# Optimization experiments

Hardware: AMD Instinct MI355X
Metric: run time of the kernel (lower is better)

The kernel has to match this reference:

```python
import jax, jax.numpy as jnp
import numpy as np
import math

B, L, D = 2, 2048, 512
D_INNER, D_STATE, D_CONV = 2 * D, 16, 4
DT_RANK = math.ceil(D / 16)  # 32


def setup_inputs() -> dict:
    key = jax.random.key(0)
    ks = jax.random.split(key, 9)
    s = 0.02
    x = jax.random.normal(ks[0], (B, L, D), dtype=jnp.float32)
    W_in = jax.random.normal(ks[1], (D, 2 * D_INNER), dtype=jnp.float32) * s
    conv_w = jax.random.normal(ks[2], (D_INNER, D_CONV), dtype=jnp.float32) * s
    conv_b = jnp.zeros((D_INNER,), dtype=jnp.float32)
    W_x = jax.random.normal(ks[3], (D_INNER, DT_RANK + 2 * D_STATE), dtype=jnp.float32) * s
    W_dt = jax.random.normal(ks[4], (DT_RANK, D_INNER), dtype=jnp.float32) * s
    b_dt = jax.random.normal(ks[5], (D_INNER,), dtype=jnp.float32) * s
    # S4D-real init: A = -[1..d_state] per channel
    A_log = jnp.log(jnp.broadcast_to(jnp.arange(1, D_STATE + 1, dtype=jnp.float32), (D_INNER, D_STATE)))
    D_param = jnp.ones((D_INNER,), dtype=jnp.float32)
    W_out = jax.random.normal(ks[6], (D_INNER, D), dtype=jnp.float32) * s
    return {"x": x, "W_in": W_in, "conv_w": conv_w, "conv_b": conv_b,
            "W_x": W_x, "W_dt": W_dt, "b_dt": b_dt, "A_log": A_log,
            "D_param": D_param, "W_out": W_out}


def _mamba(x, W_in, conv_w, conv_b, W_x, W_dt, b_dt, A_log, D_param, W_out):
    # in_proj -> [u, z]
    xz = jnp.einsum('bld,de->ble', x, W_in)
    u, z = jnp.split(xz, 2, axis=-1)  # each (B, L, d_inner)
    # depthwise causal conv1d along L
    u_c = jnp.transpose(u, (0, 2, 1))  # (B, d_inner, L)
    kern = conv_w[:, None, :]          # (d_inner, 1, d_conv)
    u_c = jax.lax.conv_general_dilated(
        u_c, kern, window_strides=(1,), padding=[(D_CONV - 1, 0)],
        feature_group_count=D_INNER,
        dimension_numbers=('NCH', 'OIH', 'NCH')) + conv_b[None, :, None]
    u = jax.nn.silu(jnp.transpose(u_c, (0, 2, 1)))  # (B, L, d_inner)
    # input-dependent dt, B, C
    x_dbl = jnp.einsum('bld,de->ble', u, W_x)
    dt_r = x_dbl[..., :DT_RANK]
    Bm = x_dbl[..., DT_RANK:DT_RANK + D_STATE]          # (B, L, d_state)
    Cm = x_dbl[..., DT_RANK + D_STATE:]                  # (B, L, d_state)
    dt = jax.nn.softplus(jnp.einsum('blr,rd->bld', dt_r, W_dt) + b_dt)  # (B, L, d_inner)
    A = -jnp.exp(A_log)  # (d_inner, d_state)

    def step(h, inp):
        dt_t, B_t, C_t, u_t = inp  # (B,d_inner), (B,d_state), (B,d_state), (B,d_inner)
        dA = jnp.exp(dt_t[:, :, None] * A)                      # (B, d_inner, d_state)
        h = h * dA + (dt_t * u_t)[:, :, None] * B_t[:, None, :]
        y = jnp.einsum('bds,bs->bd', h, C_t)
        return h, y

    h0 = jnp.zeros((B, D_INNER, D_STATE), dtype=x.dtype)
    xs = (jnp.transpose(dt, (1, 0, 2)), jnp.transpose(Bm, (1, 0, 2)),
          jnp.transpose(Cm, (1, 0, 2)), jnp.transpose(u, (1, 0, 2)))
    _, ys = jax.lax.scan(step, h0, xs)
    y = jnp.transpose(ys, (1, 0, 2)) + u * D_param  # (B, L, d_inner)
    y = y * jax.nn.silu(z)
    return jnp.einsum('bld,de->ble', y, W_out)


def reference(x, W_in, conv_w, conv_b, W_x, W_dt, b_dt, A_log, D_param, W_out):
    # MambaLayer.forward (eval): out = x + drop_path(mamba(x)); drop_path == Identity at eval
    return x + _mamba(x, W_in, conv_w, conv_b, W_x, W_dt, b_dt, A_log, D_param, W_out)
```

## Files before the change

### kernel.cpp

```cpp
#include <hip/hip_runtime.h>
#include <math.h>

#define BB 2
#define LL 2048
#define DD 512
#define DIN 1024
#define DXZ 2048
#define DSTATE 16
#define DTRANK 32
#define NDBL 64
#define ML (BB*LL)
#define LC2 64
#define NCH2 (LL/LC2)
#define CP 68

typedef __bf16 bf16_t;
typedef bf16_t bf16x8 __attribute__((ext_vector_type(8)));
typedef bf16_t bf16x4 __attribute__((ext_vector_type(4)));
typedef float f32x4 __attribute__((ext_vector_type(4)));

#define GBK 32
#define GBKP 40

__device__ __forceinline__ float fast_silu(float x) {
  return x * __builtin_amdgcn_rcpf(1.f + __builtin_amdgcn_exp2f(-1.44269504f * x));
}

template <int TM, int TN, int MODE, int CT>
__launch_bounds__(256)
__global__ void gemm_mfma(const bf16_t* __restrict__ A,
                          const bf16_t* __restrict__ Bt,
                          float* __restrict__ C, int ldc,
                          int M, int N, int K,
                          const float* __restrict__ aux) {
  __shared__ __align__(16) bf16_t As[TM * GBKP];
  __shared__ __align__(16) bf16_t Bs[TN * GBKP];
  const int tid = threadIdx.x;
  const int wid = tid >> 6, lane = tid & 63;
  const int q = lane >> 4, ln = lane & 15;
  constexpr int WM = TM / 2, WN = TN / 2;
  constexpr int FM = WM / 16, FN = WN / 16;
  const int wm = (wid >> 1) * WM, wn = (wid & 1) * WN;
  const int mBase = blockIdx.y * TM, nBase = blockIdx.x * TN;

  f32x4 acc[FM][FN] = {};

  for (int k0 = 0; k0 < K; k0 += GBK) {
#pragma unroll
    for (int i = 0; i < TM * GBK / (256 * 8); i++) {
      const int slot = tid + i * 256;
      const int m = slot >> 2, k8 = (slot & 3) * 8;
      *(bf16x8*)&As[m * GBKP + k8] =
          *(const bf16x8*)&A[(size_t)(mBase + m) * K + k0 + k8];
    }
#pragma unroll
    for (int i = 0; i < TN * GBK / (256 * 8); i++) {
      const int slot = tid + i * 256;
      const int n = slot >> 2, k8 = (slot & 3) * 8;
      *(bf16x8*)&Bs[n * GBKP + k8] =
          *(const bf16x8*)&Bt[(size_t)(nBase + n) * K + k0 + k8];
    }
    __syncthreads();
    bf16x8 af[FM], bfr[FN];
#pragma unroll
    for (int i = 0; i < FM; i++)
      af[i] = *(const bf16x8*)&As[(wm + i * 16 + ln) * GBKP + q * 8];
#pragma unroll
    for (int j = 0; j < FN; j++)
      bfr[j] = *(const bf16x8*)&Bs[(wn + j * 16 + ln) * GBKP + q * 8];
#pragma unroll
    for (int i = 0; i < FM; i++)
#pragma unroll
      for (int j = 0; j < FN; j++)
        acc[i][j] = __builtin_amdgcn_mfma_f32_16x16x32_bf16(
            af[i], bfr[j], acc[i][j], 0, 0, 0);
    __syncthreads();
  }

#pragma unroll
  for (int i = 0; i < FM; i++) {
    const int m0 = mBase + wm + i * 16 + q * 4;
#pragma unroll
    for (int j = 0; j < FN; j++) {
      const int n = nBase + wn + j * 16 + ln;
      if (CT == 1) {
        *(f32x4*)&C[(size_t)n * ldc + m0] = acc[i][j];
      } else {
#pragma unroll
        for (int r = 0; r < 4; r++) {
          float v = acc[i][j][r];
          if (MODE == 2) v += aux[(size_t)(m0 + r) * ldc + n];
          C[(size_t)(m0 + r) * ldc + n] = v;
        }
      }
    }
  }
}

__global__ void cast_bf16(const float* __restrict__ in, bf16_t* __restrict__ out,
                          int n4) {
  const int i = blockIdx.x * 256 + threadIdx.x;
  if (i >= n4) return;
  const float4 v = ((const float4*)in)[i];
  bf16x4 o = {(bf16_t)v.x, (bf16_t)v.y, (bf16_t)v.z, (bf16_t)v.w};
  ((bf16x4*)out)[i] = o;
}

__launch_bounds__(256)
__global__ void transpose_cast(const float* __restrict__ in, bf16_t* __restrict__ out,
                               int R, int C) {
  __shared__ float T[64][65];
  const int t = threadIdx.x;
  const int rB = blockIdx.y * 64, cB = blockIdx.x * 64;
  {
    const int r = t >> 4, c4 = (t & 15) * 4;
#pragma unroll
    for (int i = 0; i < 4; i++) {
      const float4 v = *(const float4*)&in[(size_t)(rB + r + i * 16) * C + cB + c4];
      T[r + i * 16][c4] = v.x;
      T[r + i * 16][c4 + 1] = v.y;
      T[r + i * 16][c4 + 2] = v.z;
      T[r + i * 16][c4 + 3] = v.w;
    }
  }
  __syncthreads();
  {
    const int c = t >> 2;
#pragma unroll
    for (int i = 0; i < 4; i++) {
      const int r0 = (t & 3) * 16 + i * 4;
      bf16x4 o = {(bf16_t)T[r0][c], (bf16_t)T[r0 + 1][c],
                  (bf16_t)T[r0 + 2][c], (bf16_t)T[r0 + 3][c]};
      *(bf16x4*)&out[(size_t)(cB + c) * R + rB + r0] = o;
    }
  }
}

template <int MODE, int AT, int CT>
__launch_bounds__(256)
__global__ void gemm_tiled(const float* __restrict__ A, int lda,
                           const float* __restrict__ B, int ldb,
                           float* __restrict__ C, int ldc,
                           int M, int N, int K,
                           const float* __restrict__ aux) {
  __shared__ float As[16][68];
  __shared__ float Bs[16][68];

  const int tid = threadIdx.x;
  const int tx = tid & 15, ty = tid >> 4;
  const int mBase = blockIdx.y * 64;
  const int nBase = blockIdx.x * 64;

  float acc[4][4] = {};

  for (int k0 = 0; k0 < K; k0 += 16) {
#pragma unroll
    for (int i = 0; i < 4; i++) {
      int idx = tid + i * 256;
      if (AT == 0) {
        int m = idx >> 4, kk = idx & 15;
        As[kk][m] = A[(size_t)(mBase + m) * lda + k0 + kk];
      } else {
        int kk = idx >> 6, m = idx & 63;
        As[kk][m] = A[(size_t)(k0 + kk) * lda + mBase + m];
      }
    }
#pragma unroll
    for (int i = 0; i < 4; i++) {
      int idx = tid + i * 256;
      int kk = idx >> 6, n = idx & 63;
      Bs[kk][n] = B[(size_t)(k0 + kk) * ldb + nBase + n];
    }
    __syncthreads();
#pragma unroll
    for (int kk = 0; kk < 16; kk++) {
      const float4 a4 = *reinterpret_cast<const float4*>(&As[kk][ty * 4]);
      const float4 b4 = *reinterpret_cast<const float4*>(&Bs[kk][tx * 4]);
      const float a[4] = {a4.x, a4.y, a4.z, a4.w};
      const float b[4] = {b4.x, b4.y, b4.z, b4.w};
#pragma unroll
      for (int i = 0; i < 4; i++)
#pragma unroll
        for (int j = 0; j < 4; j++) acc[i][j] = fmaf(a[i], b[j], acc[i][j]);
    }
    __syncthreads();
  }

  if (CT == 0) {
#pragma unroll
    for (int i = 0; i < 4; i++) {
      const int m = mBase + ty * 4 + i;
      const int n0 = nBase + tx * 4;
      float v[4];
#pragma unroll
      for (int j = 0; j < 4; j++) {
        float x = acc[i][j];
        if (MODE == 1) {
          x += aux[n0 + j];
          x = (x > 20.f) ? x
              : 0.69314718f * __builtin_amdgcn_logf(
                    1.f + __builtin_amdgcn_exp2f(x * 1.44269504f));
        }
        v[j] = x;
      }
      *reinterpret_cast<float4*>(&C[(size_t)m * ldc + n0]) =
          make_float4(v[0], v[1], v[2], v[3]);
    }
  } else {
    const int m0 = mBase + ty * 4;
#pragma unroll
    for (int j = 0; j < 4; j++) {
      const int n = nBase + tx * 4 + j;
      float v[4];
#pragma unroll
      for (int i = 0; i < 4; i++) {
        float x = acc[i][j];
        if (MODE == 1) {
          x += aux[n];
          x = (x > 20.f) ? x
              : 0.69314718f * __builtin_amdgcn_logf(
                    1.f + __builtin_amdgcn_exp2f(x * 1.44269504f));
        }
        v[i] = x;
      }
      *reinterpret_cast<float4*>(&C[(size_t)n * ldc + m0]) =
          make_float4(v[0], v[1], v[2], v[3]);
    }
  }
}

__launch_bounds__(256)
__global__ void conv_silu_T(const float* __restrict__ xzT,
                            const float* __restrict__ conv_w,
                            const float* __restrict__ conv_b,
                            float* __restrict__ uT) {
  const int idx = blockIdx.x * 256 + threadIdx.x;
  const int d = idx >> 10;
  const int ml0 = (idx & 1023) * 4;
  const int l0 = ml0 & (LL - 1);
  const float* row = xzT + (size_t)d * ML + ml0;
  const float4 Bv = *reinterpret_cast<const float4*>(row);
  float4 Av = make_float4(0.f, 0.f, 0.f, 0.f);
  if (l0 != 0) Av = *reinterpret_cast<const float4*>(row - 4);
  const float w0 = conv_w[d * 4 + 0], w1 = conv_w[d * 4 + 1];
  const float w2 = conv_w[d * 4 + 2], w3 = conv_w[d * 4 + 3];
  const float bias = conv_b[d];
  float o[4];
  o[0] = bias + w0 * Av.y + w1 * Av.z + w2 * Av.w + w3 * Bv.x;
  o[1] = bias + w0 * Av.z + w1 * Av.w + w2 * Bv.x + w3 * Bv.y;
  o[2] = bias + w0 * Av.w + w1 * Bv.x + w2 * Bv.y + w3 * Bv.z;
  o[3] = bias + w0 * Bv.x + w1 * Bv.y + w2 * Bv.z + w3 * Bv.w;
#pragma unroll
  for (int i = 0; i < 4; i++) o[i] = fast_silu(o[i]);
  *reinterpret_cast<float4*>(uT + (size_t)d * ML + ml0) =
      make_float4(o[0], o[1], o[2], o[3]);
}

__launch_bounds__(128, 3)
__global__ void scan_fused3(const float* __restrict__ dtT,
                            const float* __restrict__ uT,
                            float* __restrict__ xzT,
                            const float* __restrict__ xdbl,
                            const float* __restrict__ A_log,
                            const float* __restrict__ D_param) {
  __shared__ float dt_s[NCH2 * CP];
  __shared__ float u_s[NCH2 * CP];
  __shared__ float Pc[NCH2][DSTATE];
  __shared__ float Hc[NCH2][DSTATE];

  const int tid = threadIdx.x;
  const int c = blockIdx.x;
  const int b = c >> 10, d = c & (DIN - 1);
  const size_t rowoff = (size_t)d * ML + (size_t)b * LL;
  const float* dtrow = dtT + rowoff;
  const float* urow  = uT + rowoff;
  const float* zrow  = xzT + (size_t)(DIN + d) * ML + (size_t)b * LL;
  float* yrow = xzT + rowoff;

#pragma unroll
  for (int i = 0; i < 4; i++) {
    const int idx = (tid + i * 128) * 4;
    const int la = (idx >> 6) * CP + (idx & 63);
    *(float4*)&dt_s[la] = *(const float4*)&dtrow[idx];
    *(float4*)&u_s[la]  = *(const float4*)&urow[idx];
  }

  const int ch = tid >> 2, q = tid & 3;
  const int s0 = q * 4;
  float Al2[4];
#pragma unroll
  for (int k = 0; k < 4; k++)
    Al2[k] = -expf(A_log[d * DSTATE + s0 + k]) * 1.44269504f;
  const float* dp = dt_s + ch * CP;
  float* up = u_s + ch * CP;
  const float* BC = xdbl + ((size_t)b * LL + (size_t)ch * LC2) * NDBL + DTRANK + s0;
  __syncthreads();

  {
    float h0 = 0.f, h1 = 0.f, h2 = 0.f, h3 = 0.f, sdt = 0.f;
    float4 Bcur[4];
#pragma unroll
    for (int i = 0; i < 4; i++)
      Bcur[i] = *(const float4*)(BC + (size_t)i * NDBL);
    for (int g = 0; g < 16; g++) {
      float4 Bnxt[4];
#pragma unroll
      for (int i = 0; i < 4; i++)
        Bnxt[i] = *(const float4*)(BC + (size_t)((g + 1) * 4 + i) * NDBL);
#pragma unroll
      for (int i = 0; i < 4; i++) {
        const int l = g * 4 + i;
        const float dtv = dp[l];
        const float dtu = dtv * up[l];
        sdt += dtv;
        const float e0 = __builtin_amdgcn_exp2f(dtv * Al2[0]);
        const float e1 = __builtin_amdgcn_exp2f(dtv * Al2[1]);
        const float e2 = __builtin_amdgcn_exp2f(dtv * Al2[2]);
        const float e3 = __builtin_amdgcn_exp2f(dtv * Al2[3]);
        h0 = fmaf(h0, e0, dtu * Bcur[i].x);
        h1 = fmaf(h1, e1, dtu * Bcur[i].y);
        h2 = fmaf(h2, e2, dtu * Bcur[i].z);
        h3 = fmaf(h3, e3, dtu * Bcur[i].w);
      }
#pragma unroll
      for (int i = 0; i < 4; i++) Bcur[i] = Bnxt[i];
    }
    *(float4*)&Pc[ch][s0] = make_float4(
        __builtin_amdgcn_exp2f(Al2[0] * sdt), __builtin_amdgcn_exp2f(Al2[1] * sdt),
        __builtin_amdgcn_exp2f(Al2[2] * sdt), __builtin_amdgcn_exp2f(Al2[3] * sdt));
    *(float4*)&Hc[ch][s0] = make_float4(h0, h1, h2, h3);
  }
  __syncthreads();

  if (tid < DSTATE) {
    float h = 0.f;
#pragma unroll
    for (int k = 0; k < NCH2; k++) {
      const float Pv = Pc[k][tid], Hv = Hc[k][tid];
      Pc[k][tid] = h;
      h = fmaf(h, Pv, Hv);
    }
  }
  __syncthreads();

  {
    const float Dp = D_param[d];
    const float4 H4 = *(const float4*)&Pc[ch][s0];
    float h0 = H4.x, h1 = H4.y, h2 = H4.z, h3 = H4.w;
    float4 Bcur[4], Ccur[4];
#pragma unroll
    for (int i = 0; i < 4; i++) {
      Bcur[i] = *(const float4*)(BC + (size_t)i * NDBL);
      Ccur[i] = *(const float4*)(BC + (size_t)i * NDBL + DSTATE);
    }
    for (int g = 0; g < 16; g++) {
      float4 Bnxt[4], Cnxt[4];
#pragma unroll
      for (int i = 0; i < 4; i++) {
        Bnxt[i] = *(const float4*)(BC + (size_t)((g + 1) * 4 + i) * NDBL);
        Cnxt[i] = *(const float4*)(BC + (size_t)((g + 1) * 4 + i) * NDBL + DSTATE);
      }
#pragma unroll
      for (int i = 0; i < 4; i++) {
        const int l = g * 4 + i;
        const float dtv = dp[l];
        const float uv = up[l];
        const float dtu = dtv * uv;
        const float e0 = __builtin_amdgcn_exp2f(dtv * Al2[0]);
        const float e1 = __builtin_amdgcn_exp2f(dtv * Al2[1]);
        const float e2 = __builtin_amdgcn_exp2f(dtv * Al2[2]);
        const float e3 = __builtin_amdgcn_exp2f(dtv * Al2[3]);
        h0 = fmaf(h0, e0, dtu * Bcur[i].x);
        h1 = fmaf(h1, e1, dtu * Bcur[i].y);
        h2 = fmaf(h2, e2, dtu * Bcur[i].z);
        h3 = fmaf(h3, e3, dtu * Bcur[i].w);
        float p = fmaf(h0, Ccur[i].x,
                  fmaf(h1, Ccur[i].y, fmaf(h2, Ccur[i].z, h3 * Ccur[i].w)));
        p += __int_as_float(__builtin_amdgcn_ds_swizzle(__float_as_int(p), 0x041F));
        p += __int_as_float(__builtin_amdgcn_ds_swizzle(__float_as_int(p), 0x081F));
        if (q == (l & 3)) up[l] = p + uv * Dp;
      }
#pragma unroll
      for (int i = 0; i < 4; i++) { Bcur[i] = Bnxt[i]; Ccur[i] = Cnxt[i]; }
    }
  }
  __syncthreads();

#pragma unroll
  for (int i = 0; i < 4; i++) {
    const int idx = (tid + i * 128) * 4;
    const int la = (idx >> 6) * CP + (idx & 63);
    const float4 y4 = *(const float4*)&u_s[la];
    const float4 z4 = *(const float4*)&zrow[idx];
    float4 o;
    o.x = y4.x * fast_silu(z4.x);
    o.y = y4.y * fast_silu(z4.y);
    o.z = y4.z * fast_silu(z4.z);
    o.w = y4.w * fast_silu(z4.w);
    *(float4*)&yrow[idx] = o;
  }
}

extern "C" void kernel_launch(void* const* d_in, const int* in_sizes, int n_in,
                              void* d_out, int out_size, void* d_ws, size_t ws_size,
                              hipStream_t stream) {
  const float* x      = (const float*)d_in[0];
  const float* W_in   = (const float*)d_in[1];
  const float* conv_w = (const float*)d_in[2];
  const float* conv_b = (const float*)d_in[3];
  const float* W_x    = (const float*)d_in[4];
  const float* W_dt   = (const float*)d_in[5];
  const float* b_dt   = (const float*)d_in[6];
  const float* A_log  = (const float*)d_in[7];
  const float* D_par  = (const float*)d_in[8];
  const float* W_out  = (const float*)d_in[9];
  float* out = (float*)d_out;

  char* ws = (char*)d_ws;
  float* xzT   = (float*)(ws);
  float* uT    = (float*)(ws + (size_t)ML * DXZ * 4);
  float* x_dbl = (float*)(ws + (size_t)ML * (DXZ + DIN) * 4);
  char* dtT_b  = ws + (size_t)ML * (DXZ + DIN + NDBL) * 4;
  float* dtT   = (float*)dtT_b;
  bf16_t* u_b  = (bf16_t*)dtT_b;
  bf16_t* y_b  = (bf16_t*)(dtT_b + (size_t)ML * DIN * 2);
  char* extra  = ws + (size_t)ML * (DXZ + DIN + NDBL + DIN) * 4;
  bf16_t* x_b      = (bf16_t*)(extra);
  bf16_t* W_inT_b  = (bf16_t*)(extra + (size_t)ML * DD * 2);
  bf16_t* W_outT_b = (bf16_t*)(extra + (size_t)ML * DD * 2 + (size_t)DXZ * DD * 2);
  bf16_t* W_xT_b   = (bf16_t*)(extra + (size_t)ML * DD * 2 + (size_t)DXZ * DD * 2
                               + (size_t)DD * DIN * 2);

  cast_bf16<<<(ML * DD / 4) / 256, 256, 0, stream>>>(x, x_b, ML * DD / 4);
  transpose_cast<<<dim3(DXZ / 64, DD / 64), 256, 0, stream>>>(W_in, W_inT_b, DD, DXZ);
  transpose_cast<<<dim3(1, DIN / 64), 256, 0, stream>>>(W_x, W_xT_b, DIN, NDBL);
  transpose_cast<<<dim3(DD / 64, DIN / 64), 256, 0, stream>>>(W_out, W_outT_b, DIN, DD);

  gemm_mfma<128, 128, 0, 1><<<dim3(DXZ / 128, ML / 128), 256, 0, stream>>>(
      x_b, W_inT_b, xzT, ML, ML, DXZ, DD, nullptr);

  conv_silu_T<<<(DIN * (ML / 4)) / 256, 256, 0, stream>>>(xzT, conv_w, conv_b, uT);

  transpose_cast<<<dim3(ML / 64, DIN / 64), 256, 0, stream>>>(uT, u_b, DIN, ML);

  gemm_mfma<64, 64, 0, 0><<<dim3(1, ML / 64), 256, 0, stream>>>(
      u_b, W_xT_b, x_dbl, NDBL, ML, NDBL, DIN, nullptr);

  gemm_tiled<1, 0, 1><<<dim3(DIN / 64, ML / 64), 256, 0, stream>>>(
      x_dbl, NDBL, W_dt, DIN, dtT, ML, ML, DIN, DTRANK, b_dt);

  scan_fused3<<<BB * DIN, 128, 0, stream>>>(dtT, uT, xzT, x_dbl, A_log, D_par);

  transpose_cast<<<dim3(ML / 64, DIN / 64), 256, 0, stream>>>(xzT, y_b, DIN, ML);

  gemm_mfma<128, 64, 2, 0><<<dim3(DD / 64, ML / 128), 256, 0, stream>>>(
      y_b, W_outT_b, out, DD, ML, DD, DIN, x);
}
```

Baseline: 224.5 us.

## Restructure chunked scan into single local pass plus carry-in correction

The old kernel scanned each chunk twice: once to get chunk-end states and once with the carried-in state to produce outputs. Now each chunk is scanned once from a zero state, producing local outputs and prefix sums of dt. The cross-chunk carry is added afterwards as a correction sum over states of h_in·exp(A·cumdt)·C. This drops one full sequential recurrence pass. In exchange it adds 16 exp2 calls per timestep in the correction, more C reloads from global memory, and more register pressure.

```diff
diff --git a/kernel.cpp b/kernel.cpp
--- a/kernel.cpp
+++ b/kernel.cpp
@@ -257,7 +257,7 @@
 }
 
 __launch_bounds__(128, 3)
-__global__ void scan_fused3(const float* __restrict__ dtT,
+__global__ void scan_fused4(const float* __restrict__ dtT,
                             const float* __restrict__ uT,
                             float* __restrict__ xzT,
                             const float* __restrict__ xdbl,
@@ -267,6 +267,7 @@
   __shared__ float u_s[NCH2 * CP];
   __shared__ float Pc[NCH2][DSTATE];
   __shared__ float Hc[NCH2][DSTATE];
+  __shared__ float Al2s[DSTATE];
 
   const int tid = threadIdx.x;
   const int c = blockIdx.x;
@@ -277,6 +278,9 @@
   const float* zrow  = xzT + (size_t)(DIN + d) * ML + (size_t)b * LL;
   float* yrow = xzT + rowoff;
 
+  if (tid < DSTATE)
+    Al2s[tid] = -expf(A_log[d * DSTATE + tid]) * 1.44269504f;
+
 #pragma unroll
   for (int i = 0; i < 4; i++) {
     const int idx = (tid + i * 128) * 4;
@@ -287,66 +291,19 @@
 
   const int ch = tid >> 2, q = tid & 3;
   const int s0 = q * 4;
-  float Al2[4];
-#pragma unroll
-  for (int k = 0; k < 4; k++)
-    Al2[k] = -expf(A_log[d * DSTATE + s0 + k]) * 1.44269504f;
   const float* dp = dt_s + ch * CP;
+  float* dpw = dt_s + ch * CP;
   float* up = u_s + ch * CP;
   const float* BC = xdbl + ((size_t)b * LL + (size_t)ch * LC2) * NDBL + DTRANK + s0;
   __syncthreads();
 
-  {
-    float h0 = 0.f, h1 = 0.f, h2 = 0.f, h3 = 0.f, sdt = 0.f;
-    float4 Bcur[4];
-#pragma unroll
-    for (int i = 0; i < 4; i++)
-      Bcur[i] = *(const float4*)(BC + (size_t)i * NDBL);
-    for (int g = 0; g < 16; g++) {
-      float4 Bnxt[4];
-#pragma unroll
-      for (int i = 0; i < 4; i++)
-        Bnxt[i] = *(const float4*)(BC + (size_t)((g + 1) * 4 + i) * NDBL);
-#pragma unroll
-      for (int i = 0; i < 4; i++) {
-        const int l = g * 4 + i;
-        const float dtv = dp[l];
-        const float dtu = dtv * up[l];
-        sdt += dtv;
-        const float e0 = __builtin_amdgcn_exp2f(dtv * Al2[0]);
-        const float e1 = __builtin_amdgcn_exp2f(dtv * Al2[1]);
-        const float e2 = __builtin_amdgcn_exp2f(dtv * Al2[2]);
-        const float e3 = __builtin_amdgcn_exp2f(dtv * Al2[3]);
-        h0 = fmaf(h0, e0, dtu * Bcur[i].x);
-        h1 = fmaf(h1, e1, dtu * Bcur[i].y);
-        h2 = fmaf(h2, e2, dtu * Bcur[i].z);
-        h3 = fmaf(h3, e3, dtu * Bcur[i].w);
-      }
-#pragma unroll
-      for (int i = 0; i < 4; i++) Bcur[i] = Bnxt[i];
-    }
-    *(float4*)&Pc[ch][s0] = make_float4(
-        __builtin_amdgcn_exp2f(Al2[0] * sdt), __builtin_amdgcn_exp2f(Al2[1] * sdt),
-        __builtin_amdgcn_exp2f(Al2[2] * sdt), __builtin_amdgcn_exp2f(Al2[3] * sdt));
-    *(float4*)&Hc[ch][s0] = make_float4(h0, h1, h2, h3);
-  }
-  __syncthreads();
-
-  if (tid < DSTATE) {
-    float h = 0.f;
-#pragma unroll
-    for (int k = 0; k < NCH2; k++) {
-      const float Pv = Pc[k][tid], Hv = Hc[k][tid];
-      Pc[k][tid] = h;
-      h = fmaf(h, Pv, Hv);
-    }
-  }
-  __syncthreads();
+  float Al2[4];
+#pragma unroll
+  for (int k = 0; k < 4; k++) Al2[k] = Al2s[s0 + k];
 
   {
     const float Dp = D_param[d];
-    const float4 H4 = *(const float4*)&Pc[ch][s0];
-    float h0 = H4.x, h1 = H4.y, h2 = H4.z, h3 = H4.w;
+    float h0 = 0.f, h1 = 0.f, h2 = 0.f, h3 = 0.f, sdt = 0.f;
     float4 Bcur[4], Ccur[4];
 #pragma unroll
     for (int i = 0; i < 4; i++) {
@@ -366,6 +323,7 @@
         const float dtv = dp[l];
         const float uv = up[l];
         const float dtu = dtv * uv;
+        sdt += dtv;
         const float e0 = __builtin_amdgcn_exp2f(dtv * Al2[0]);
         const float e1 = __builtin_amdgcn_exp2f(dtv * Al2[1]);
         const float e2 = __builtin_amdgcn_exp2f(dtv * Al2[2]);
@@ -378,10 +336,78 @@
                   fmaf(h1, Ccur[i].y, fmaf(h2, Ccur[i].z, h3 * Ccur[i].w)));
         p += __int_as_float(__builtin_amdgcn_ds_swizzle(__float_as_int(p), 0x041F));
         p += __int_as_float(__builtin_amdgcn_ds_swizzle(__float_as_int(p), 0x081F));
-        if (q == (l & 3)) up[l] = p + uv * Dp;
+        if (q == i) {
+          up[l] = fmaf(uv, Dp, p);
+          dpw[l] = sdt;
+        }
       }
 #pragma unroll
       for (int i = 0; i < 4; i++) { Bcur[i] = Bnxt[i]; Ccur[i] = Cnxt[i]; }
+    }
+    *(float4*)&Pc[ch][s0] = make_float4(
+        __builtin_amdgcn_exp2f(Al2[0] * sdt), __builtin_amdgcn_exp2f(Al2[1] * sdt),
+        __builtin_amdgcn_exp2f(Al2[2] * sdt), __builtin_amdgcn_exp2f(Al2[3] * sdt));
+    *(float4*)&Hc[ch][s0] = make_float4(h0, h1, h2, h3);
+  }
+  __syncthreads();
+
+  if (tid < DSTATE) {
+    float h = 0.f;
+#pragma unroll
+    for (int k = 0; k < NCH2; k++) {
+      const float Pv = Pc[k][tid], Hv = Hc[k][tid];
+      Pc[k][tid] = h;
+      h = fmaf(h, Pv, Hv);
+    }
+  }
+  __syncthreads();
+
+  {
+    float Hin[16], Af[16];
+#pragma unroll
+    for (int s = 0; s < 4; s++) {
+      const float4 hv = *(const float4*)&Pc[ch][s * 4];
+      Hin[s * 4 + 0] = hv.x; Hin[s * 4 + 1] = hv.y;
+      Hin[s * 4 + 2] = hv.z; Hin[s * 4 + 3] = hv.w;
+      const float4 av = *(const float4*)&Al2s[s * 4];
+      Af[s * 4 + 0] = av.x; Af[s * 4 + 1] = av.y;
+      Af[s * 4 + 2] = av.z; Af[s * 4 + 3] = av.w;
+    }
+    const float* Crow = xdbl + ((size_t)b * LL + (size_t)ch * LC2) * NDBL
+                        + DTRANK + DSTATE;
+#pragma unroll
+    for (int j = 0; j < 4; j++) {
+      float o[4];
+#pragma unroll
+      for (int jj = 0; jj < 4; jj++) {
+        const int l = q * 16 + j * 4 + jj;
+        const float S = dp[l];
+        const float* Cl = Crow + (size_t)l * NDBL;
+        const float4 C0 = *(const float4*)(Cl);
+        const float4 C1 = *(const float4*)(Cl + 4);
+        const float4 C2 = *(const float4*)(Cl + 8);
+        const float4 C3 = *(const float4*)(Cl + 12);
+        float pa = up[l];
+        float pb = 0.f, pcc = 0.f, pd = 0.f;
+        pa = fmaf(Hin[0]  * __builtin_amdgcn_exp2f(Af[0]  * S), C0.x, pa);
+        pb = fmaf(Hin[1]  * __builtin_amdgcn_exp2f(Af[1]  * S), C0.y, pb);
+        pcc = fmaf(Hin[2] * __builtin_amdgcn_exp2f(Af[2]  * S), C0.z, pcc);
+        pd = fmaf(Hin[3]  * __builtin_amdgcn_exp2f(Af[3]  * S), C0.w, pd);
+        pa = fmaf(Hin[4]  * __builtin_amdgcn_exp2f(Af[4]  * S), C1.x, pa);
+        pb = fmaf(Hin[5]  * __builtin_amdgcn_exp2f(Af[5]  * S), C1.y, pb);
+        pcc = fmaf(Hin[6] * __builtin_amdgcn_exp2f(Af[6]  * S), C1.z, pcc);
+        pd = fmaf(Hin[7]  * __builtin_amdgcn_exp2f(Af[7]  * S), C1.w, pd);
+        pa = fmaf(Hin[8]  * __builtin_amdgcn_exp2f(Af[8]  * S), C2.x, pa);
+        pb = fmaf(Hin[9]  * __builtin_amdgcn_exp2f(Af[9]  * S), C2.y, pb);
+        pcc = fmaf(Hin[10] * __builtin_amdgcn_exp2f(Af[10] * S), C2.z, pcc);
+        pd = fmaf(Hin[11] * __builtin_amdgcn_exp2f(Af[11] * S), C2.w, pd);
+        pa = fmaf(Hin[12] * __builtin_amdgcn_exp2f(Af[12] * S), C3.x, pa);
+        pb = fmaf(Hin[13] * __builtin_amdgcn_exp2f(Af[13] * S), C3.y, pb);
+        pcc = fmaf(Hin[14] * __builtin_amdgcn_exp2f(Af[14] * S), C3.z, pcc);
+        pd = fmaf(Hin[15] * __builtin_amdgcn_exp2f(Af[15] * S), C3.w, pd);
+        o[jj] = (pa + pb) + (pcc + pd);
+      }
+      *(float4*)&up[q * 16 + j * 4] = make_float4(o[0], o[1], o[2], o[3]);
     }
   }
   __syncthreads();
@@ -449,7 +475,7 @@
   gemm_tiled<1, 0, 1><<<dim3(DIN / 64, ML / 64), 256, 0, stream>>>(
       x_dbl, NDBL, W_dt, DIN, dtT, ML, ML, DIN, DTRANK, b_dt);
 
-  scan_fused3<<<BB * DIN, 128, 0, stream>>>(dtT, uT, xzT, x_dbl, A_log, D_par);
+  scan_fused4<<<BB * DIN, 128, 0, stream>>>(dtT, uT, xzT, x_dbl, A_log, D_par);
 
   transpose_cast<<<dim3(ML / 64, DIN / 64), 256, 0, stream>>>(xzT, y_b, DIN, ML);
 
```

Result: slower. 253.6 us (+13.0%).

## Restructure scan so each thread owns all 16 states of one chunk

Applied to the files above, without the earlier changes.

The chunked selective scan now maps each thread to one 64-step chunk of one channel and keeps all 16 state values in registers, with four channels per block. The old mapping split the states across 4 lanes and combined them with swizzle reductions. dt, u and z are read directly from global memory instead of being staged in shared memory, and the silu(z) gating is fused into the second pass. This removes the shared-memory staging, the cross-lane swizzles and a block sync. In exchange each thread uses more registers, the B/C loads become per-thread strided global reads, and dt/u reads are no longer coalesced across lanes (each lane reads its own 64-element chunk).

```diff
diff --git a/kernel.cpp b/kernel.cpp
--- a/kernel.cpp
+++ b/kernel.cpp
@@ -12,7 +12,6 @@
 #define ML (BB*LL)
 #define LC2 64
 #define NCH2 (LL/LC2)
-#define CP 68
 
 typedef __bf16 bf16_t;
 typedef bf16_t bf16x8 __attribute__((ext_vector_type(8)));
@@ -256,148 +255,152 @@
       make_float4(o[0], o[1], o[2], o[3]);
 }
 
-__launch_bounds__(128, 3)
-__global__ void scan_fused3(const float* __restrict__ dtT,
+__launch_bounds__(128)
+__global__ void scan_fused5(const float* __restrict__ dtT,
                             const float* __restrict__ uT,
                             float* __restrict__ xzT,
                             const float* __restrict__ xdbl,
                             const float* __restrict__ A_log,
                             const float* __restrict__ D_param) {
-  __shared__ float dt_s[NCH2 * CP];
-  __shared__ float u_s[NCH2 * CP];
-  __shared__ float Pc[NCH2][DSTATE];
-  __shared__ float Hc[NCH2][DSTATE];
+  __shared__ __align__(16) float Pc[4][32][20];
+  __shared__ __align__(16) float Hc[4][32][20];
 
   const int tid = threadIdx.x;
-  const int c = blockIdx.x;
-  const int b = c >> 10, d = c & (DIN - 1);
-  const size_t rowoff = (size_t)d * ML + (size_t)b * LL;
+  const int dg = tid >> 5, ch = tid & 31;
+  const int blk = blockIdx.x;
+  const int b = blk >> 8;
+  const int d = ((blk & 255) << 2) + dg;
+  const size_t rowoff = (size_t)d * ML + (size_t)b * LL + (size_t)ch * LC2;
   const float* dtrow = dtT + rowoff;
   const float* urow  = uT + rowoff;
-  const float* zrow  = xzT + (size_t)(DIN + d) * ML + (size_t)b * LL;
+  const float* zrow  = xzT + (size_t)(DIN + d) * ML + (size_t)b * LL + (size_t)ch * LC2;
   float* yrow = xzT + rowoff;
-
-#pragma unroll
-  for (int i = 0; i < 4; i++) {
-    const int idx = (tid + i * 128) * 4;
-    const int la = (idx >> 6) * CP + (idx & 63);
-    *(float4*)&dt_s[la] = *(const float4*)&dtrow[idx];
-    *(float4*)&u_s[la]  = *(const float4*)&urow[idx];
-  }
-
-  const int ch = tid >> 2, q = tid & 3;
-  const int s0 = q * 4;
-  float Al2[4];
-#pragma unroll
-  for (int k = 0; k < 4; k++)
-    Al2[k] = -expf(A_log[d * DSTATE + s0 + k]) * 1.44269504f;
-  const float* dp = dt_s + ch * CP;
-  float* up = u_s + ch * CP;
-  const float* BC = xdbl + ((size_t)b * LL + (size_t)ch * LC2) * NDBL + DTRANK + s0;
-  __syncthreads();
+  const float* BC = xdbl + ((size_t)b * LL + (size_t)ch * LC2) * NDBL + DTRANK;
+
+  float Al2[16];
+#pragma unroll
+  for (int s4 = 0; s4 < 4; s4++) {
+    const f32x4 a4 = *(const f32x4*)&A_log[(size_t)d * DSTATE + s4 * 4];
+#pragma unroll
+    for (int j = 0; j < 4; j++)
+      Al2[s4 * 4 + j] =
+          -__builtin_amdgcn_exp2f(a4[j] * 1.44269504f) * 1.44269504f;
+  }
+
+  float h[16];
+#pragma unroll
+  for (int s = 0; s < 16; s++) h[s] = 0.f;
 
   {
-    float h0 = 0.f, h1 = 0.f, h2 = 0.f, h3 = 0.f, sdt = 0.f;
-    float4 Bcur[4];
-#pragma unroll
-    for (int i = 0; i < 4; i++)
-      Bcur[i] = *(const float4*)(BC + (size_t)i * NDBL);
+    float sdt = 0.f;
+    f32x4 dt4 = *(const f32x4*)dtrow;
+    f32x4 u4  = *(const f32x4*)urow;
+    f32x4 Bc[4];
+#pragma unroll
+    for (int j = 0; j < 4; j++) Bc[j] = *(const f32x4*)(BC + j * 4);
     for (int g = 0; g < 16; g++) {
-      float4 Bnxt[4];
-#pragma unroll
-      for (int i = 0; i < 4; i++)
-        Bnxt[i] = *(const float4*)(BC + (size_t)((g + 1) * 4 + i) * NDBL);
+      const f32x4 dt4n = *(const f32x4*)(dtrow + (size_t)(g + 1) * 4);
+      const f32x4 u4n  = *(const f32x4*)(urow + (size_t)(g + 1) * 4);
 #pragma unroll
       for (int i = 0; i < 4; i++) {
         const int l = g * 4 + i;
-        const float dtv = dp[l];
-        const float dtu = dtv * up[l];
+        f32x4 Bn[4];
+#pragma unroll
+        for (int j = 0; j < 4; j++)
+          Bn[j] = *(const f32x4*)(BC + (size_t)(l + 1) * NDBL + j * 4);
+        const float dtv = dt4[i];
+        const float uv  = u4[i];
+        const float dtu = dtv * uv;
         sdt += dtv;
-        const float e0 = __builtin_amdgcn_exp2f(dtv * Al2[0]);
-        const float e1 = __builtin_amdgcn_exp2f(dtv * Al2[1]);
-        const float e2 = __builtin_amdgcn_exp2f(dtv * Al2[2]);
-        const float e3 = __builtin_amdgcn_exp2f(dtv * Al2[3]);
-        h0 = fmaf(h0, e0, dtu * Bcur[i].x);
-        h1 = fmaf(h1, e1, dtu * Bcur[i].y);
-        h2 = fmaf(h2, e2, dtu * Bcur[i].z);
-        h3 = fmaf(h3, e3, dtu * Bcur[i].w);
-      }
-#pragma unroll
-      for (int i = 0; i < 4; i++) Bcur[i] = Bnxt[i];
-    }
-    *(float4*)&Pc[ch][s0] = make_float4(
-        __builtin_amdgcn_exp2f(Al2[0] * sdt), __builtin_amdgcn_exp2f(Al2[1] * sdt),
-        __builtin_amdgcn_exp2f(Al2[2] * sdt), __builtin_amdgcn_exp2f(Al2[3] * sdt));
-    *(float4*)&Hc[ch][s0] = make_float4(h0, h1, h2, h3);
+#pragma unroll
+        for (int s = 0; s < 16; s++) {
+          const float e = __builtin_amdgcn_exp2f(dtv * Al2[s]);
+          h[s] = fmaf(h[s], e, dtu * Bc[s >> 2][s & 3]);
+        }
+#pragma unroll
+        for (int j = 0; j < 4; j++) Bc[j] = Bn[j];
+      }
+      dt4 = dt4n; u4 = u4n;
+    }
+#pragma unroll
+    for (int s4 = 0; s4 < 4; s4++) {
+      f32x4 hv, pv;
+#pragma unroll
+      for (int j = 0; j < 4; j++) {
+        hv[j] = h[s4 * 4 + j];
+        pv[j] = __builtin_amdgcn_exp2f(Al2[s4 * 4 + j] * sdt);
+      }
+      *(f32x4*)&Hc[dg][ch][s4 * 4] = hv;
+      *(f32x4*)&Pc[dg][ch][s4 * 4] = pv;
+    }
   }
   __syncthreads();
 
-  if (tid < DSTATE) {
-    float h = 0.f;
+  if (tid < 64) {
+    const int pg = tid >> 4, s = tid & 15;
+    float hh = 0.f;
 #pragma unroll
     for (int k = 0; k < NCH2; k++) {
-      const float Pv = Pc[k][tid], Hv = Hc[k][tid];
-      Pc[k][tid] = h;
-      h = fmaf(h, Pv, Hv);
+      const float Pv = Pc[pg][k][s], Hv = Hc[pg][k][s];
+      Pc[pg][k][s] = hh;
+      hh = fmaf(hh, Pv, Hv);
     }
   }
   __syncthreads();
 
   {
     const float Dp = D_param[d];
-    const float4 H4 = *(const float4*)&Pc[ch][s0];
-    float h0 = H4.x, h1 = H4.y, h2 = H4.z, h3 = H4.w;
-    float4 Bcur[4], Ccur[4];
-#pragma unroll
-    for (int i = 0; i < 4; i++) {
-      Bcur[i] = *(const float4*)(BC + (size_t)i * NDBL);
-      Ccur[i] = *(const float4*)(BC + (size_t)i * NDBL + DSTATE);
+#pragma unroll
+    for (int s4 = 0; s4 < 4; s4++) {
+      const f32x4 hv = *(const f32x4*)&Pc[dg][ch][s4 * 4];
+#pragma unroll
+      for (int j = 0; j < 4; j++) h[s4 * 4 + j] = hv[j];
+    }
+    f32x4 dt4 = *(const f32x4*)dtrow;
+    f32x4 u4  = *(const f32x4*)urow;
+    f32x4 z4  = *(const f32x4*)zrow;
+    f32x4 Bc[4], Cc[4];
+#pragma unroll
+    for (int j = 0; j < 4; j++) {
+      Bc[j] = *(const f32x4*)(BC + j * 4);
+      Cc[j] = *(const f32x4*)(BC + DSTATE + j * 4);
     }
     for (int g = 0; g < 16; g++) {
-      float4 Bnxt[4], Cnxt[4];
-#pragma unroll
-      for (int i = 0; i < 4; i++) {
-        Bnxt[i] = *(const float4*)(BC + (size_t)((g + 1) * 4 + i) * NDBL);
-        Cnxt[i] = *(const float4*)(BC + (size_t)((g + 1) * 4 + i) * NDBL + DSTATE);
-      }
+      const f32x4 dt4n = *(const f32x4*)(dtrow + (size_t)(g + 1) * 4);
+      const f32x4 u4n  = *(const f32x4*)(urow + (size_t)(g + 1) * 4);
+      const f32x4 z4n  = *(const f32x4*)(zrow + (size_t)(g + 1) * 4);
+      f32x4 y4;
 #pragma unroll
       for (int i = 0; i < 4; i++) {
         const int l = g * 4 + i;
-        const float dtv = dp[l];
-        const float uv = up[l];
+        f32x4 Bn[4], Cn[4];
+#pragma unroll
+        for (int j = 0; j < 4; j++) {
+          Bn[j] = *(const f32x4*)(BC + (size_t)(l + 1) * NDBL + j * 4);
+          Cn[j] = *(const f32x4*)(BC + (size_t)(l + 1) * NDBL + DSTATE + j * 4);
+        }
+        const float dtv = dt4[i];
+        const float uv  = u4[i];
         const float dtu = dtv * uv;
-        const float e0 = __builtin_amdgcn_exp2f(dtv * Al2[0]);
-        const float e1 = __builtin_amdgcn_exp2f(dtv * Al2[1]);
-        const float e2 = __builtin_amdgcn_exp2f(dtv * Al2[2]);
-        const float e3 = __builtin_amdgcn_exp2f(dtv * Al2[3]);
-        h0 = fmaf(h0, e0, dtu * Bcur[i].x);
-        h1 = fmaf(h1, e1, dtu * Bcur[i].y);
-        h2 = fmaf(h2, e2, dtu * Bcur[i].z);
-        h3 = fmaf(h3, e3, dtu * Bcur[i].w);
-        float p = fmaf(h0, Ccur[i].x,
-                  fmaf(h1, Ccur[i].y, fmaf(h2, Ccur[i].z, h3 * Ccur[i].w)));
-        p += __int_as_float(__builtin_amdgcn_ds_swizzle(__float_as_int(p), 0x041F));
-        p += __int_as_float(__builtin_amdgcn_ds_swizzle(__float_as_int(p), 0x081F));
-        if (q == (l & 3)) up[l] = p + uv * Dp;
-      }
-#pragma unroll
-      for (int i = 0; i < 4; i++) { Bcur[i] = Bnxt[i]; Ccur[i] = Cnxt[i]; }
-    }
-  }
-  __syncthreads();
-
-#pragma unroll
-  for (int i = 0; i < 4; i++) {
-    const int idx = (tid + i * 128) * 4;
-    const int la = (idx >> 6) * CP + (idx & 63);
-    const float4 y4 = *(const float4*)&u_s[la];
-    const float4 z4 = *(const float4*)&zrow[idx];
-    float4 o;
-    o.x = y4.x * fast_silu(z4.x);
-    o.y = y4.y * fast_silu(z4.y);
-    o.z = y4.z * fast_silu(z4.z);
-    o.w = y4.w * fast_silu(z4.w);
-    *(float4*)&yrow[idx] = o;
+        float p0 = 0.f, p1 = 0.f, p2 = 0.f, p3 = 0.f;
+#pragma unroll
+        for (int s = 0; s < 16; s++) {
+          const float e = __builtin_amdgcn_exp2f(dtv * Al2[s]);
+          h[s] = fmaf(h[s], e, dtu * Bc[s >> 2][s & 3]);
+          const float cs = Cc[s >> 2][s & 3];
+          if ((s & 3) == 0)      p0 = fmaf(h[s], cs, p0);
+          else if ((s & 3) == 1) p1 = fmaf(h[s], cs, p1);
+          else if ((s & 3) == 2) p2 = fmaf(h[s], cs, p2);
+          else                   p3 = fmaf(h[s], cs, p3);
+        }
+        const float yv = ((p0 + p1) + (p2 + p3)) + uv * Dp;
+        y4[i] = yv * fast_silu(z4[i]);
+#pragma unroll
+        for (int j = 0; j < 4; j++) { Bc[j] = Bn[j]; Cc[j] = Cn[j]; }
+      }
+      *(f32x4*)(yrow + (size_t)g * 4) = y4;
+      dt4 = dt4n; u4 = u4n; z4 = z4n;
+    }
   }
 }
 
@@ -449,7 +452,7 @@
   gemm_tiled<1, 0, 1><<<dim3(DIN / 64, ML / 64), 256, 0, stream>>>(
       x_dbl, NDBL, W_dt, DIN, dtT, ML, ML, DIN, DTRANK, b_dt);
 
-  scan_fused3<<<BB * DIN, 128, 0, stream>>>(dtT, uT, xzT, x_dbl, A_log, D_par);
+  scan_fused5<<<BB * DIN / 4, 128, 0, stream>>>(dtT, uT, xzT, x_dbl, A_log, D_par);
 
   transpose_cast<<<dim3(ML / 64, DIN / 64), 256, 0, stream>>>(xzT, y_b, DIN, ML);
 
```

New measurement: 283.3 us. 1.26x slower.
